# Optimization experiments

Measured on AMD Instinct MI355X. Metric: run time of the kernel, lower is better.

The kernel has to match this reference:

```python
import jax, jax.numpy as jnp
import numpy as np

NUM_HEADS = 4
HID = 64
NUM_LAYERS = 3
NEG_SLOPE = 0.2  # PyG GATConv default


def setup_inputs() -> dict:
    key = jax.random.key(0)
    ks = jax.random.split(key, 6)
    B, N, D = 64, 512, 64
    return {
        "embeddings": jax.random.normal(ks[0], (B, N, D), jnp.float32),
        "lin_w": jax.random.normal(ks[1], (NUM_LAYERS, NUM_HEADS * HID, D), jnp.float32) * 0.1,
        "att_src": jax.random.normal(ks[2], (NUM_LAYERS, NUM_HEADS, HID), jnp.float32) * 0.1,
        "att_dst": jax.random.normal(ks[3], (NUM_LAYERS, NUM_HEADS, HID), jnp.float32) * 0.1,
        "conv_b": jnp.zeros((NUM_LAYERS, HID), jnp.float32),
        "readout_w": jax.random.normal(ks[4], (D, HID), jnp.float32) * 0.1,
        "readout_b": jnp.zeros((D,), jnp.float32),
    }


def reference(embeddings, lin_w, att_src, att_dst, conv_b, readout_w, readout_b):
    # Graph is fully connected (combinations + reversed) and PyG GATConv adds
    # self-loops by default -> attention softmax over ALL nodes j for each i.
    B, N, _ = embeddings.shape
    x = embeddings
    for l in range(NUM_LAYERS):
        h = jnp.einsum('bnd,od->bno', x, lin_w[l]).reshape(B, N, NUM_HEADS, HID)  # [B,N,H,C]
        a_src = jnp.einsum('bnhc,hc->bnh', h, att_src[l])  # per source node j
        a_dst = jnp.einsum('bnhc,hc->bnh', h, att_dst[l])  # per target node i
        e = a_dst[:, :, None, :] + a_src[:, None, :, :]    # [B,i,j,H]
        e = jnp.where(e >= 0, e, NEG_SLOPE * e)            # LeakyReLU(0.2)
        alpha = jax.nn.softmax(e, axis=2)                  # softmax over neighbors j
        out = jnp.einsum('bijh,bjhc->bihc', alpha, h).mean(axis=2) + conv_b[l]  # concat=False -> head mean
        x = jax.nn.relu(out)
    pooled = x.mean(axis=1)                                # mean over nodes
    return pooled @ readout_w.T + readout_b                # [B, D]
```

## Files before the change

### kernel.cpp

```cpp
#include <hip/hip_runtime.h>
#include <math.h>


using short8  = __attribute__((ext_vector_type(8))) short;
using floatx4 = __attribute__((ext_vector_type(4))) float;

__device__ inline unsigned short f2bf(float f) {
    union { float f; unsigned u; } v; v.f = f;
    unsigned u = v.u + 0x7FFFu + ((v.u >> 16) & 1u);
    return (unsigned short)(u >> 16);
}
__device__ inline float bf2f(unsigned short s) {
    union { float f; unsigned u; } v; v.u = ((unsigned)s) << 16;
    return v.f;
}

__device__ inline void cvt8(const float4 a, const float4 b, short8& hi, short8& lo) {
    float f[8] = {a.x, a.y, a.z, a.w, b.x, b.y, b.z, b.w};
    short8 H, L;
#pragma unroll
    for (int i = 0; i < 8; ++i) {
        unsigned short h = f2bf(f[i]);
        H[i] = (short)h;
        L[i] = (short)f2bf(f[i] - bf2f(h));
    }
    hi = H; lo = L;
}

__global__ __launch_bounds__(256) void linprep_kernel(const float* __restrict__ x,
                                                      const float* __restrict__ W,
                                                      const float* __restrict__ att_src,
                                                      const float* __restrict__ att_dst,
                                                      float* __restrict__ hT,
                                                      int* __restrict__ g_rank,
                                                      float2* __restrict__ g_E12,
                                                      float2* __restrict__ g_ab,
                                                      int* __restrict__ g_k) {
    __shared__ unsigned short WH[64 * 72], WL[64 * 72];
    __shared__ float sA[512], dA[512];
    __shared__ int   s_idxE[512];
    __shared__ float z1suf[513], z2pre[513];
    __shared__ float wred[8];

    const int t  = threadIdx.x;
    const int r8 = blockIdx.x & 7;
    const int q  = blockIdx.x >> 3;
    const int ct = q & 3;
    const int b  = ((q >> 2) << 3) | r8;
    const int bh = b * 4 + ct;
    const int c0 = ct * 64;

#pragma unroll
    for (int qq = 0; qq < 4; ++qq) {
        int f = qq * 256 + t;
        int wrow = f >> 4, d4 = f & 15;
        float4 v = *(const float4*)(W + (size_t)(c0 + wrow) * 64 + d4 * 4);
        unsigned short h0 = f2bf(v.x), h1 = f2bf(v.y), h2 = f2bf(v.z), h3 = f2bf(v.w);
        ushort4 hi = make_ushort4(h0, h1, h2, h3);
        ushort4 lo = make_ushort4(f2bf(v.x - bf2f(h0)), f2bf(v.y - bf2f(h1)),
                                  f2bf(v.z - bf2f(h2)), f2bf(v.w - bf2f(h3)));
        *(ushort4*)&WH[wrow * 72 + d4 * 4] = hi;
        *(ushort4*)&WL[wrow * 72 + d4 * 4] = lo;
    }
    __syncthreads();

    const int lane = t & 63, wv = t >> 6;
    const int mrow = lane & 15, quad = lane >> 4;

    short8 bhf[4][2], blf[4][2];
#pragma unroll
    for (int g = 0; g < 4; ++g)
#pragma unroll
        for (int kk = 0; kk < 2; ++kk) {
            int ko = kk * 32 + quad * 8;
            bhf[g][kk] = *(const short8*)&WH[(g * 16 + mrow) * 72 + ko];
            blf[g][kk] = *(const short8*)&WL[(g * 16 + mrow) * 72 + ko];
        }
    float as_g[4], ad_g[4];
#pragma unroll
    for (int g = 0; g < 4; ++g) {
        as_g[g] = att_src[c0 + g * 16 + mrow];
        ad_g[g] = att_dst[c0 + g * 16 + mrow];
    }

    const float* xbase = x + (size_t)(b * 512 + mrow) * 64 + quad * 8;
    float4 nxa = *(const float4*)(xbase + (size_t)wv * 1024);
    float4 nxb = *(const float4*)(xbase + (size_t)wv * 1024 + 4);
    float4 nxc = *(const float4*)(xbase + (size_t)wv * 1024 + 32);
    float4 nxd = *(const float4*)(xbase + (size_t)wv * 1024 + 36);

#pragma unroll 1
    for (int tl = wv; tl < 32; tl += 4) {
        float4 xa = nxa, xb = nxb, xc = nxc, xd = nxd;
        if (tl + 4 < 32) {
            const float* nb = xbase + (size_t)(tl + 4) * 1024;
            nxa = *(const float4*)(nb);
            nxb = *(const float4*)(nb + 4);
            nxc = *(const float4*)(nb + 32);
            nxd = *(const float4*)(nb + 36);
        }
        short8 ah0, al0, ah1, al1;
        cvt8(xa, xb, ah0, al0);
        cvt8(xc, xd, ah1, al1);

        floatx4 acc[4];
#pragma unroll
        for (int g = 0; g < 4; ++g) {
            floatx4 a = {0.f, 0.f, 0.f, 0.f};
            a = __builtin_amdgcn_mfma_f32_16x16x32_bf16(ah0, bhf[g][0], a, 0, 0, 0);
            a = __builtin_amdgcn_mfma_f32_16x16x32_bf16(ah1, bhf[g][1], a, 0, 0, 0);
            a = __builtin_amdgcn_mfma_f32_16x16x32_bf16(ah0, blf[g][0], a, 0, 0, 0);
            a = __builtin_amdgcn_mfma_f32_16x16x32_bf16(ah1, blf[g][1], a, 0, 0, 0);
            a = __builtin_amdgcn_mfma_f32_16x16x32_bf16(al0, bhf[g][0], a, 0, 0, 0);
            a = __builtin_amdgcn_mfma_f32_16x16x32_bf16(al1, bhf[g][1], a, 0, 0, 0);
            acc[g] = a;
        }

        const int r0 = b * 512 + tl * 16;
#pragma unroll
        for (int g = 0; g < 4; ++g) {
            *(float4*)&hT[(size_t)(ct * 64 + g * 16 + mrow) * 32768 + r0 + quad * 4] =
                make_float4(acc[g][0], acc[g][1], acc[g][2], acc[g][3]);
        }

        float ps[4], pd[4];
#pragma unroll
        for (int reg = 0; reg < 4; ++reg) {
            ps[reg] = acc[0][reg] * as_g[0] + acc[1][reg] * as_g[1]
                    + acc[2][reg] * as_g[2] + acc[3][reg] * as_g[3];
            pd[reg] = acc[0][reg] * ad_g[0] + acc[1][reg] * ad_g[1]
                    + acc[2][reg] * ad_g[2] + acc[3][reg] * ad_g[3];
        }
#pragma unroll
        for (int m = 1; m <= 8; m <<= 1) {
#pragma unroll
            for (int reg = 0; reg < 4; ++reg) {
                ps[reg] += __shfl_xor(ps[reg], m, 64);
                pd[reg] += __shfl_xor(pd[reg], m, 64);
            }
        }
        if (mrow < 4) {
            sA[tl * 16 + quad * 4 + mrow] = ps[mrow];
            dA[tl * 16 + quad * 4 + mrow] = pd[mrow];
        }
    }
    __syncthreads();

    const int wid = t >> 6;

    float dreg[2];
    for (int rr = 0; rr < 2; ++rr) dreg[rr] = dA[t + rr * 256];

    float v0 = sA[2 * t], v1 = sA[2 * t + 1];
    int id0 = 2 * t, id1 = 2 * t + 1;
    for (int k = 2; k <= 512; k <<= 1) {
        for (int j = k >> 1; j >= 1; j >>= 1) {
            bool asc = ((t & (k >> 1)) == 0);
            if (j == 1) {
                bool sw = asc ? (v0 > v1) : (v0 < v1);
                if (sw) { float tv = v0; v0 = v1; v1 = tv; int ti = id0; id0 = id1; id1 = ti; }
            } else if (j <= 64) {
                int m = j >> 1;
                float w0 = __shfl_xor(v0, m, 64);
                int  wi0 = __shfl_xor(id0, m, 64);
                float w1 = __shfl_xor(v1, m, 64);
                int  wi1 = __shfl_xor(id1, m, 64);
                bool low = ((t & m) == 0);
                bool wantmin = (low == asc);
                if (wantmin ? (w0 < v0) : (w0 > v0)) { v0 = w0; id0 = wi0; }
                if (wantmin ? (w1 < v1) : (w1 > v1)) { v1 = w1; id1 = wi1; }
            } else {
                int m = j >> 1;
                sA[2 * t] = v0; sA[2 * t + 1] = v1;
                s_idxE[2 * t] = id0; s_idxE[2 * t + 1] = id1;
                __syncthreads();
                int tp = t ^ m;
                float w0 = sA[2 * tp], w1 = sA[2 * tp + 1];
                int wi0 = s_idxE[2 * tp], wi1 = s_idxE[2 * tp + 1];
                bool low = ((t & m) == 0);
                bool wantmin = (low == asc);
                if (wantmin ? (w0 < v0) : (w0 > v0)) { v0 = w0; id0 = wi0; }
                if (wantmin ? (w1 < v1) : (w1 > v1)) { v1 = w1; id1 = wi1; }
                __syncthreads();
            }
        }
    }

    sA[2 * t] = v0; sA[2 * t + 1] = v1;
    __syncthreads();
    const float M = sA[511];
    float e1_0 = __expf(v0 - M), e1_1 = __expf(v1 - M);
    float e2_0 = __expf(0.2f * (v0 - M)), e2_1 = __expf(0.2f * (v1 - M));
    {
        const int base = bh * 512;
        g_E12[base + id0] = make_float2(e1_0, e2_0);
        g_E12[base + id1] = make_float2(e1_1, e2_1);
        g_rank[base + id0] = 2 * t;  g_rank[base + id1] = 2 * t + 1;
    }

    float S1 = e1_0 + e1_1, S2 = e2_0 + e2_1;
    float i1 = S1, i2 = S2;
    for (int off = 1; off < 64; off <<= 1) {
        float u1 = __shfl_up(i1, off, 64);
        float u2 = __shfl_up(i2, off, 64);
        if (lane >= off) { i1 += u1; i2 += u2; }
    }
    if (lane == 63) { wred[wid] = i1; wred[4 + wid] = i2; }
    __syncthreads();
    float off1 = 0.f, off2 = 0.f;
    for (int w = 0; w < wid; ++w) { off1 += wred[w]; off2 += wred[4 + w]; }
    const float T1 = wred[0] + wred[1] + wred[2] + wred[3];
    const float T2 = wred[4] + wred[5] + wred[6] + wred[7];
    float pre1 = off1 + i1 - S1;
    float pre2 = off2 + i2 - S2;
    z1suf[2 * t] = T1 - pre1;
    z1suf[2 * t + 1] = T1 - pre1 - e1_0;
    z2pre[2 * t] = pre2;
    z2pre[2 * t + 1] = pre2 + e2_0;
    if (t == 0) { z1suf[512] = 0.f; z2pre[512] = T2; }
    __syncthreads();

    for (int rr = 0; rr < 2; ++rr) {
        int i = t + rr * 256;
        float d = dreg[rr];
        int lo = 0, hi = 512;
        while (lo < hi) {
            int mid = (lo + hi) >> 1;
            if (d + sA[mid] >= 0.f) hi = mid; else lo = mid + 1;
        }
        int k = lo;
        float g = d + M;
        float G = (g >= 0.f) ? g : 0.2f * g;
        float al = __expf(g - G);
        float be = __expf(0.2f * g - G);
        float Z = al * z1suf[k] + be * z2pre[k];
        float inv = 1.0f / Z;
        g_ab[bh * 512 + i] = make_float2(al * inv, be * inv);
        g_k[bh * 512 + i]  = k;
    }
}

__global__ __launch_bounds__(256) void attn_agg_fin(const float* __restrict__ hT,
                                                    const int* __restrict__ g_rank,
                                                    const float2* __restrict__ g_E12,
                                                    const float2* __restrict__ g_ab,
                                                    const int* __restrict__ g_k,
                                                    const float* __restrict__ bias,
                                                    float* __restrict__ x) {
    const int r8 = blockIdx.x & 7;
    const int qq = blockIdx.x >> 3;
    const int cg = qq & 31;
    const int b  = ((qq >> 5) << 3) | r8;
    const int c0 = cg * 2;
    const int t = threadIdx.x;
    const int lane = t & 63, wv = t >> 6;

    __shared__ float A1[4][2][512], A2[4][2][512];
    __shared__ float tots[4][2];

    {
        const int bh = b * 4 + wv;
        const int base = bh * 512;
        const float* hTb = hT + (size_t)(wv * 64 + c0) * 32768 + (size_t)b * 512;
#pragma unroll
        for (int it = 0; it < 8; ++it) {
            int j = it * 64 + lane;
            int rk = g_rank[base + j];
            float2 e12 = g_E12[base + j];
            float h0 = hTb[j];
            float h1 = hTb[32768 + j];
            int pk = ((rk & 7) << 6) | (rk >> 3);
            A1[wv][0][pk] = e12.x * h0;  A2[wv][0][pk] = e12.y * h0;
            A1[wv][1][pk] = e12.x * h1;  A2[wv][1][pk] = e12.y * h1;
        }
#pragma unroll
        for (int cc = 0; cc < 2; ++cc) {
            float v1[8], v2[8];
#pragma unroll
            for (int i = 0; i < 8; ++i) {
                v1[i] = A1[wv][cc][i * 64 + lane];
                v2[i] = A2[wv][cc][i * 64 + lane];
            }
            float s1 = 0.f, s2 = 0.f;
#pragma unroll
            for (int i = 0; i < 8; ++i) { s1 += v1[i]; s2 += v2[i]; }
            float suf = s1;
#pragma unroll
            for (int off = 1; off < 64; off <<= 1) {
                float u = __shfl_down(suf, off, 64);
                if (lane + off < 64) suf += u;
            }
            float run = suf - s1;
            float pre = s2;
#pragma unroll
            for (int off = 1; off < 64; off <<= 1) {
                float u = __shfl_up(pre, off, 64);
                if (lane >= off) pre += u;
            }
            float run2 = pre - s2;
            if (lane == 63) tots[wv][cc] = pre;
#pragma unroll
            for (int i = 7; i >= 0; --i) { run += v1[i]; v1[i] = run; }
#pragma unroll
            for (int i = 0; i < 8; ++i) { float tv = v2[i]; v2[i] = run2; run2 += tv; }
#pragma unroll
            for (int i = 0; i < 8; ++i) {
                A1[wv][cc][i * 64 + lane] = v1[i];
                A2[wv][cc][i * 64 + lane] = v2[i];
            }
        }
    }
    __syncthreads();

    const float bv0 = bias[c0], bv1 = bias[c0 + 1];
#pragma unroll
    for (int rr = 0; rr < 2; ++rr) {
        const int i = t + rr * 256;
        float a0 = 0.f, a1 = 0.f;
#pragma unroll
        for (int head = 0; head < 4; ++head) {
            const int base = (b * 4 + head) * 512;
            float2 ab = g_ab[base + i];
            int k = g_k[base + i];
            if (k < 512) {
                int pk = ((k & 7) << 6) | (k >> 3);
                a0 += ab.x * A1[head][0][pk] + ab.y * A2[head][0][pk];
                a1 += ab.x * A1[head][1][pk] + ab.y * A2[head][1][pk];
            } else {
                a0 += ab.y * tots[head][0];
                a1 += ab.y * tots[head][1];
            }
        }
        float2 o = make_float2(fmaxf(0.25f * a0 + bv0, 0.f),
                               fmaxf(0.25f * a1 + bv1, 0.f));
        *(float2*)&x[(size_t)(b * 512 + i) * 64 + c0] = o;
    }
}

__global__ __launch_bounds__(256) void readout_kernel(const float* __restrict__ x,
                                                      const float* __restrict__ rw,
                                                      const float* __restrict__ rb,
                                                      float* __restrict__ out) {
    __shared__ float red[4][64];
    __shared__ float pooled[64];
    int b = blockIdx.x, t = threadIdx.x;
    int c = t & 63, q = t >> 6;
    float acc = 0.f;
    for (int n = q; n < 512; n += 4) acc += x[((size_t)b * 512 + n) * 64 + c];
    red[q][c] = acc;
    __syncthreads();
    if (t < 64) pooled[t] = (red[0][t] + red[1][t] + red[2][t] + red[3][t]) * (1.0f / 512.0f);
    __syncthreads();
    if (t < 64) {
        float a = rb[t];
        for (int cc = 0; cc < 64; ++cc) a += pooled[cc] * rw[t * 64 + cc];
        out[b * 64 + t] = a;
    }
}

extern "C" void kernel_launch(void* const* d_in, const int* in_sizes, int n_in,
                              void* d_out, int out_size, void* d_ws, size_t ws_size,
                              hipStream_t stream) {
    const float* emb       = (const float*)d_in[0];
    const float* lin_w     = (const float*)d_in[1];
    const float* att_src   = (const float*)d_in[2];
    const float* att_dst   = (const float*)d_in[3];
    const float* conv_b    = (const float*)d_in[4];
    const float* readout_w = (const float*)d_in[5];
    const float* readout_b = (const float*)d_in[6];
    float* out = (float*)d_out;

    float* ws   = (float*)d_ws;
    float* xbuf = ws;
    float* hT   = ws + 2097152;
    float* meta = ws + 10485760;

    int*    g_rank = (int*)meta;
    float2* g_E12  = (float2*)(meta + 131072);
    float2* g_ab   = (float2*)(meta + 393216);
    int*    g_k    = (int*)(meta + 655360);

    for (int l = 0; l < 3; ++l) {
        const float* xin = (l == 0) ? emb : xbuf;
        linprep_kernel<<<256, 256, 0, stream>>>(xin, lin_w + (size_t)l * 16384,
                                                att_src + l * 256, att_dst + l * 256,
                                                hT, g_rank, g_E12, g_ab, g_k);
        attn_agg_fin<<<2048, 256, 0, stream>>>(hT, g_rank, g_E12, g_ab, g_k,
                                               conv_b + l * 64, xbuf);
    }
    readout_kernel<<<64, 256, 0, stream>>>(xbuf, readout_w, readout_b, out);
}
```

Baseline: 231.6 us.

## Double linprep block size and pack rank/exp and alpha/beta/k into float4 records

The linprep kernel now launches 512 threads per block, so the MFMA projection loop runs over 8 waves instead of 4. The sort and softmax-prep stages are kept on the first 256 threads through an active-thread guard. Rank, exp values, alpha/beta and the split index k, which were four separate arrays, are now packed into two float4 arrays. The aim is to get more latency hiding in the projection phase and fewer separate gather loads in the aggregation kernel. In exchange, half the threads idle during the sort, and each stored record is padded, so more bytes are written.

```diff
diff --git a/kernel.cpp b/kernel.cpp
--- a/kernel.cpp
+++ b/kernel.cpp
@@ -27,15 +27,13 @@
     hi = H; lo = L;
 }
 
-__global__ __launch_bounds__(256) void linprep_kernel(const float* __restrict__ x,
+__global__ __launch_bounds__(512) void linprep_kernel(const float* __restrict__ x,
                                                       const float* __restrict__ W,
                                                       const float* __restrict__ att_src,
                                                       const float* __restrict__ att_dst,
                                                       float* __restrict__ hT,
-                                                      int* __restrict__ g_rank,
-                                                      float2* __restrict__ g_E12,
-                                                      float2* __restrict__ g_ab,
-                                                      int* __restrict__ g_k) {
+                                                      float4* __restrict__ g_rE,
+                                                      float4* __restrict__ g_abk) {
     __shared__ unsigned short WH[64 * 72], WL[64 * 72];
     __shared__ float sA[512], dA[512];
     __shared__ int   s_idxE[512];
@@ -51,8 +49,8 @@
     const int c0 = ct * 64;
 
 #pragma unroll
-    for (int qq = 0; qq < 4; ++qq) {
-        int f = qq * 256 + t;
+    for (int qq = 0; qq < 2; ++qq) {
+        int f = qq * 512 + t;
         int wrow = f >> 4, d4 = f & 15;
         float4 v = *(const float4*)(W + (size_t)(c0 + wrow) * 64 + d4 * 4);
         unsigned short h0 = f2bf(v.x), h1 = f2bf(v.y), h2 = f2bf(v.z), h3 = f2bf(v.w);
@@ -90,10 +88,10 @@
     float4 nxd = *(const float4*)(xbase + (size_t)wv * 1024 + 36);
 
 #pragma unroll 1
-    for (int tl = wv; tl < 32; tl += 4) {
+    for (int tl = wv; tl < 32; tl += 8) {
         float4 xa = nxa, xb = nxb, xc = nxc, xd = nxd;
-        if (tl + 4 < 32) {
-            const float* nb = xbase + (size_t)(tl + 4) * 1024;
+        if (tl + 8 < 32) {
+            const float* nb = xbase + (size_t)(tl + 8) * 1024;
             nxa = *(const float4*)(nb);
             nxb = *(const float4*)(nb + 4);
             nxc = *(const float4*)(nb + 32);
@@ -146,105 +144,124 @@
     }
     __syncthreads();
 
+    const bool act = (t < 256);
     const int wid = t >> 6;
 
-    float dreg[2];
-    for (int rr = 0; rr < 2; ++rr) dreg[rr] = dA[t + rr * 256];
-
-    float v0 = sA[2 * t], v1 = sA[2 * t + 1];
-    int id0 = 2 * t, id1 = 2 * t + 1;
+    float dreg[2] = {0.f, 0.f};
+    if (act) {
+        dreg[0] = dA[t];
+        dreg[1] = dA[t + 256];
+    }
+
+    float v0 = 0.f, v1 = 0.f;
+    int id0 = 0, id1 = 0;
+    if (act) { v0 = sA[2 * t]; v1 = sA[2 * t + 1]; id0 = 2 * t; id1 = 2 * t + 1; }
+
     for (int k = 2; k <= 512; k <<= 1) {
         for (int j = k >> 1; j >= 1; j >>= 1) {
             bool asc = ((t & (k >> 1)) == 0);
             if (j == 1) {
-                bool sw = asc ? (v0 > v1) : (v0 < v1);
-                if (sw) { float tv = v0; v0 = v1; v1 = tv; int ti = id0; id0 = id1; id1 = ti; }
+                if (act) {
+                    bool sw = asc ? (v0 > v1) : (v0 < v1);
+                    if (sw) { float tv = v0; v0 = v1; v1 = tv; int ti = id0; id0 = id1; id1 = ti; }
+                }
             } else if (j <= 64) {
-                int m = j >> 1;
-                float w0 = __shfl_xor(v0, m, 64);
-                int  wi0 = __shfl_xor(id0, m, 64);
-                float w1 = __shfl_xor(v1, m, 64);
-                int  wi1 = __shfl_xor(id1, m, 64);
-                bool low = ((t & m) == 0);
-                bool wantmin = (low == asc);
-                if (wantmin ? (w0 < v0) : (w0 > v0)) { v0 = w0; id0 = wi0; }
-                if (wantmin ? (w1 < v1) : (w1 > v1)) { v1 = w1; id1 = wi1; }
+                if (act) {
+                    int m = j >> 1;
+                    float w0 = __shfl_xor(v0, m, 64);
+                    int  wi0 = __shfl_xor(id0, m, 64);
+                    float w1 = __shfl_xor(v1, m, 64);
+                    int  wi1 = __shfl_xor(id1, m, 64);
+                    bool low = ((t & m) == 0);
+                    bool wantmin = (low == asc);
+                    if (wantmin ? (w0 < v0) : (w0 > v0)) { v0 = w0; id0 = wi0; }
+                    if (wantmin ? (w1 < v1) : (w1 > v1)) { v1 = w1; id1 = wi1; }
+                }
             } else {
                 int m = j >> 1;
-                sA[2 * t] = v0; sA[2 * t + 1] = v1;
-                s_idxE[2 * t] = id0; s_idxE[2 * t + 1] = id1;
+                if (act) {
+                    sA[2 * t] = v0; sA[2 * t + 1] = v1;
+                    s_idxE[2 * t] = id0; s_idxE[2 * t + 1] = id1;
+                }
                 __syncthreads();
-                int tp = t ^ m;
-                float w0 = sA[2 * tp], w1 = sA[2 * tp + 1];
-                int wi0 = s_idxE[2 * tp], wi1 = s_idxE[2 * tp + 1];
-                bool low = ((t & m) == 0);
-                bool wantmin = (low == asc);
-                if (wantmin ? (w0 < v0) : (w0 > v0)) { v0 = w0; id0 = wi0; }
-                if (wantmin ? (w1 < v1) : (w1 > v1)) { v1 = w1; id1 = wi1; }
+                if (act) {
+                    int tp = t ^ m;
+                    float w0 = sA[2 * tp], w1 = sA[2 * tp + 1];
+                    int wi0 = s_idxE[2 * tp], wi1 = s_idxE[2 * tp + 1];
+                    bool low = ((t & m) == 0);
+                    bool wantmin = (low == asc);
+                    if (wantmin ? (w0 < v0) : (w0 > v0)) { v0 = w0; id0 = wi0; }
+                    if (wantmin ? (w1 < v1) : (w1 > v1)) { v1 = w1; id1 = wi1; }
+                }
                 __syncthreads();
             }
         }
     }
 
-    sA[2 * t] = v0; sA[2 * t + 1] = v1;
+    if (act) { sA[2 * t] = v0; sA[2 * t + 1] = v1; }
     __syncthreads();
     const float M = sA[511];
-    float e1_0 = __expf(v0 - M), e1_1 = __expf(v1 - M);
-    float e2_0 = __expf(0.2f * (v0 - M)), e2_1 = __expf(0.2f * (v1 - M));
-    {
+
+    float e1_0 = 0.f, e1_1 = 0.f, e2_0 = 0.f, e2_1 = 0.f;
+    if (act) {
+        e1_0 = __expf(v0 - M);  e1_1 = __expf(v1 - M);
+        e2_0 = __expf(0.2f * (v0 - M));  e2_1 = __expf(0.2f * (v1 - M));
         const int base = bh * 512;
-        g_E12[base + id0] = make_float2(e1_0, e2_0);
-        g_E12[base + id1] = make_float2(e1_1, e2_1);
-        g_rank[base + id0] = 2 * t;  g_rank[base + id1] = 2 * t + 1;
+        g_rE[base + id0] = make_float4(__int_as_float(2 * t),     e1_0, e2_0, 0.f);
+        g_rE[base + id1] = make_float4(__int_as_float(2 * t + 1), e1_1, e2_1, 0.f);
     }
 
     float S1 = e1_0 + e1_1, S2 = e2_0 + e2_1;
     float i1 = S1, i2 = S2;
-    for (int off = 1; off < 64; off <<= 1) {
-        float u1 = __shfl_up(i1, off, 64);
-        float u2 = __shfl_up(i2, off, 64);
-        if (lane >= off) { i1 += u1; i2 += u2; }
-    }
-    if (lane == 63) { wred[wid] = i1; wred[4 + wid] = i2; }
-    __syncthreads();
-    float off1 = 0.f, off2 = 0.f;
-    for (int w = 0; w < wid; ++w) { off1 += wred[w]; off2 += wred[4 + w]; }
-    const float T1 = wred[0] + wred[1] + wred[2] + wred[3];
-    const float T2 = wred[4] + wred[5] + wred[6] + wred[7];
-    float pre1 = off1 + i1 - S1;
-    float pre2 = off2 + i2 - S2;
-    z1suf[2 * t] = T1 - pre1;
-    z1suf[2 * t + 1] = T1 - pre1 - e1_0;
-    z2pre[2 * t] = pre2;
-    z2pre[2 * t + 1] = pre2 + e2_0;
-    if (t == 0) { z1suf[512] = 0.f; z2pre[512] = T2; }
-    __syncthreads();
-
-    for (int rr = 0; rr < 2; ++rr) {
-        int i = t + rr * 256;
-        float d = dreg[rr];
-        int lo = 0, hi = 512;
-        while (lo < hi) {
-            int mid = (lo + hi) >> 1;
-            if (d + sA[mid] >= 0.f) hi = mid; else lo = mid + 1;
-        }
-        int k = lo;
-        float g = d + M;
-        float G = (g >= 0.f) ? g : 0.2f * g;
-        float al = __expf(g - G);
-        float be = __expf(0.2f * g - G);
-        float Z = al * z1suf[k] + be * z2pre[k];
-        float inv = 1.0f / Z;
-        g_ab[bh * 512 + i] = make_float2(al * inv, be * inv);
-        g_k[bh * 512 + i]  = k;
+    if (act) {
+        for (int off = 1; off < 64; off <<= 1) {
+            float u1 = __shfl_up(i1, off, 64);
+            float u2 = __shfl_up(i2, off, 64);
+            if (lane >= off) { i1 += u1; i2 += u2; }
+        }
+        if (lane == 63) { wred[wid] = i1; wred[4 + wid] = i2; }
+    }
+    __syncthreads();
+    if (act) {
+        float off1 = 0.f, off2 = 0.f;
+        for (int w = 0; w < wid; ++w) { off1 += wred[w]; off2 += wred[4 + w]; }
+        const float T1 = wred[0] + wred[1] + wred[2] + wred[3];
+        const float T2 = wred[4] + wred[5] + wred[6] + wred[7];
+        float pre1 = off1 + i1 - S1;
+        float pre2 = off2 + i2 - S2;
+        z1suf[2 * t] = T1 - pre1;
+        z1suf[2 * t + 1] = T1 - pre1 - e1_0;
+        z2pre[2 * t] = pre2;
+        z2pre[2 * t + 1] = pre2 + e2_0;
+        if (t == 0) { z1suf[512] = 0.f; z2pre[512] = T2; }
+    }
+    __syncthreads();
+
+    if (act) {
+        for (int rr = 0; rr < 2; ++rr) {
+            int i = t + rr * 256;
+            float d = dreg[rr];
+            int lo = 0, hi = 512;
+            while (lo < hi) {
+                int mid = (lo + hi) >> 1;
+                if (d + sA[mid] >= 0.f) hi = mid; else lo = mid + 1;
+            }
+            int k = lo;
+            float g = d + M;
+            float G = (g >= 0.f) ? g : 0.2f * g;
+            float al = __expf(g - G);
+            float be = __expf(0.2f * g - G);
+            float Z = al * z1suf[k] + be * z2pre[k];
+            float inv = 1.0f / Z;
+            g_abk[bh * 512 + i] = make_float4(al * inv, be * inv,
+                                              __int_as_float(k), 0.f);
+        }
     }
 }
 
 __global__ __launch_bounds__(256) void attn_agg_fin(const float* __restrict__ hT,
-                                                    const int* __restrict__ g_rank,
-                                                    const float2* __restrict__ g_E12,
-                                                    const float2* __restrict__ g_ab,
-                                                    const int* __restrict__ g_k,
+                                                    const float4* __restrict__ g_rE,
+                                                    const float4* __restrict__ g_abk,
                                                     const float* __restrict__ bias,
                                                     float* __restrict__ x) {
     const int r8 = blockIdx.x & 7;
@@ -265,13 +282,13 @@
 #pragma unroll
         for (int it = 0; it < 8; ++it) {
             int j = it * 64 + lane;
-            int rk = g_rank[base + j];
-            float2 e12 = g_E12[base + j];
+            float4 rE = g_rE[base + j];
+            int rk = __float_as_int(rE.x);
             float h0 = hTb[j];
             float h1 = hTb[32768 + j];
             int pk = ((rk & 7) << 6) | (rk >> 3);
-            A1[wv][0][pk] = e12.x * h0;  A2[wv][0][pk] = e12.y * h0;
-            A1[wv][1][pk] = e12.x * h1;  A2[wv][1][pk] = e12.y * h1;
+            A1[wv][0][pk] = rE.y * h0;  A2[wv][0][pk] = rE.z * h0;
+            A1[wv][1][pk] = rE.y * h1;  A2[wv][1][pk] = rE.z * h1;
         }
 #pragma unroll
         for (int cc = 0; cc < 2; ++cc) {
@@ -320,15 +337,15 @@
 #pragma unroll
         for (int head = 0; head < 4; ++head) {
             const int base = (b * 4 + head) * 512;
-            float2 ab = g_ab[base + i];
-            int k = g_k[base + i];
+            float4 abk = g_abk[base + i];
+            int k = __float_as_int(abk.z);
             if (k < 512) {
                 int pk = ((k & 7) << 6) | (k >> 3);
-                a0 += ab.x * A1[head][0][pk] + ab.y * A2[head][0][pk];
-                a1 += ab.x * A1[head][1][pk] + ab.y * A2[head][1][pk];
+                a0 += abk.x * A1[head][0][pk] + abk.y * A2[head][0][pk];
+                a1 += abk.x * A1[head][1][pk] + abk.y * A2[head][1][pk];
             } else {
-                a0 += ab.y * tots[head][0];
-                a1 += ab.y * tots[head][1];
+                a0 += abk.y * tots[head][0];
+                a1 += abk.y * tots[head][1];
             }
         }
         float2 o = make_float2(fmaxf(0.25f * a0 + bv0, 0.f),
@@ -375,17 +392,15 @@
     float* hT   = ws + 2097152;
     float* meta = ws + 10485760;
 
-    int*    g_rank = (int*)meta;
-    float2* g_E12  = (float2*)(meta + 131072);
-    float2* g_ab   = (float2*)(meta + 393216);
-    int*    g_k    = (int*)(meta + 655360);
+    float4* g_rE  = (float4*)meta;
+    float4* g_abk = (float4*)(meta + 524288);
 
     for (int l = 0; l < 3; ++l) {
         const float* xin = (l == 0) ? emb : xbuf;
-        linprep_kernel<<<256, 256, 0, stream>>>(xin, lin_w + (size_t)l * 16384,
+        linprep_kernel<<<256, 512, 0, stream>>>(xin, lin_w + (size_t)l * 16384,
                                                 att_src + l * 256, att_dst + l * 256,
-                                                hT, g_rank, g_E12, g_ab, g_k);
-        attn_agg_fin<<<2048, 256, 0, stream>>>(hT, g_rank, g_E12, g_ab, g_k,
+                                                hT, g_rE, g_abk);
+        attn_agg_fin<<<2048, 256, 0, stream>>>(hT, g_rE, g_abk,
                                                conv_b + l * 64, xbuf);
     }
     readout_kernel<<<64, 256, 0, stream>>>(xbuf, readout_w, readout_b, out);
```

New measurement: 229.2 us. About the same (-1.1%).
